# Kernel tuning notes

Measured on AMD Instinct MI355X. Metric: run time of the kernel, lower is better.

The kernel has to match this reference:

```python
import jax, jax.numpy as jnp
import numpy as np

NUM_HEADS = 16
TEMPERATURE = 1.0


def setup_inputs() -> dict:
    key = jax.random.key(0)
    ks = jax.random.split(key, 6)
    B, H = 2048, 2048
    return {
        "hidden_states": jax.random.normal(ks[0], (B, H), dtype=jnp.float32),
        "attention_mask": jnp.ones((B,), dtype=bool),
        "Wq": jax.random.normal(ks[1], (H, H), dtype=jnp.float32) * 0.02,
        "Wk": jax.random.normal(ks[2], (H, H), dtype=jnp.float32) * 0.02,
        "Wv": jax.random.normal(ks[3], (H, H), dtype=jnp.float32) * 0.02,
        "Wo": jax.random.normal(ks[4], (H, H), dtype=jnp.float32) * 0.02,
        "scale_param": jnp.full((1,), -3.0, dtype=jnp.float32),
    }


def reference(hidden_states, attention_mask, Wq, Wk, Wv, Wo, scale_param):
    B, H = hidden_states.shape
    nh = NUM_HEADS
    hd = H // nh
    # projections (torch Linear: x @ W.T), reshape to [heads, batch, head_dim]
    q = (hidden_states @ Wq.T).reshape(B, nh, hd).transpose(1, 0, 2)
    k = (hidden_states @ Wk.T).reshape(B, nh, hd).transpose(1, 0, 2)
    v = (hidden_states @ Wv.T).reshape(B, nh, hd).transpose(1, 0, 2)
    # cross-batch scores [heads, B, B]
    scores = jnp.einsum('hqd,hkd->hqk', q, k) / (hd ** 0.5 * TEMPERATURE)
    neg_inf = jnp.float32(-jnp.inf)
    eye = jnp.eye(B, dtype=bool)  # exclude self-attention (diagonal)
    scores = jnp.where(eye[None, :, :], neg_inf, scores)
    scores = jnp.where(attention_mask[None, None, :], scores, neg_inf)
    attn = jax.nn.softmax(scores, axis=-1)
    attn = jnp.nan_to_num(attn, nan=0.0)  # rows fully masked -> 0 (dropout=0 is identity)
    ctx = jnp.einsum('hqk,hkd->hqd', attn, v)  # [heads, B, head_dim]
    ctx = ctx.transpose(1, 0, 2).reshape(B, H)
    cross = ctx @ Wo.T
    scale = jax.nn.sigmoid(scale_param[0])
    return hidden_states + scale * cross
```

## Files before the change

kernel.cpp:

```cpp
#include <hip/hip_runtime.h>

typedef __bf16 bf16;
typedef __attribute__((ext_vector_type(8))) __bf16 bf16x8;
typedef __attribute__((ext_vector_type(4))) float f32x4;
typedef __attribute__((ext_vector_type(4))) short s16x4;

#define HDIM 2048

__device__ __forceinline__ void glds16(const void* g, void* l) {
  __builtin_amdgcn_global_load_lds((const __attribute__((address_space(1))) void*)g,
                                   (__attribute__((address_space(3))) void*)l,
                                   16, 0, 0);
}

#define MFMA16(a, b, c) __builtin_amdgcn_mfma_f32_16x16x32_bf16(a, b, c, 0, 0, 0)

__global__ __launch_bounds__(256) void cvt5(
    const float* __restrict__ s0, const float* __restrict__ s1,
    const float* __restrict__ s2, const float* __restrict__ s3,
    const float* __restrict__ s4,
    bf16* __restrict__ d0, bf16* __restrict__ d1, bf16* __restrict__ d2,
    bf16* __restrict__ d3, bf16* __restrict__ d4) {
  const float* s; bf16* d;
  switch (blockIdx.y) {
    case 0: s = s0; d = d0; break;
    case 1: s = s1; d = d1; break;
    case 2: s = s2; d = d2; break;
    case 3: s = s3; d = d3; break;
    default: s = s4; d = d4; break;
  }
  const size_t base = (size_t)blockIdx.x * 4096 + (threadIdx.x << 2);
  for (int i = 0; i < 4; i++) {
    const float4 v = *(const float4*)(s + base + i * 1024);
    union { bf16 h[4]; s16x4 s4v; } u;
    u.h[0] = (bf16)v.x; u.h[1] = (bf16)v.y; u.h[2] = (bf16)v.z; u.h[3] = (bf16)v.w;
    *(s16x4*)(d + base + i * 1024) = u.s4v;
  }
}

__device__ __forceinline__ void gemm128_core(const bf16* __restrict__ A,
                                             const bf16* __restrict__ B,
                                             int rowBase, int colBase,
                                             f32x4 acc[4][4],
                                             bf16* ldsA, bf16* ldsB) {
  const int t = threadIdx.x;
  const int w = t >> 6, l = t & 63;
  const int wr = (w >> 1) << 6, wc = (w & 1) << 6;
  const int lr = l & 15, lq = l >> 4;

  for (int mi = 0; mi < 4; mi++)
    for (int ni = 0; ni < 4; ni++)
      for (int r = 0; r < 4; r++) acc[mi][ni][r] = 0.f;

  const int sRow = (w << 4) + (l >> 2);
  const int sCol = (l & 3) << 3;
  const bf16* gA = A + (size_t)(rowBase + sRow) * HDIM + sCol;
  const bf16* gB = B + (size_t)(colBase + sRow) * HDIM + sCol;
  bf16* lA = ldsA + (w << 9);
  bf16* lB = ldsB + (w << 9);

  for (int k0 = 0; k0 < HDIM; k0 += 32) {
    glds16(gA, lA);
    glds16(gA + (size_t)64 * HDIM, lA + 2048);
    glds16(gB, lB);
    glds16(gB + (size_t)64 * HDIM, lB + 2048);
    gA += 32; gB += 32;
    __syncthreads();

    bf16x8 af[4], bfr[4];
    for (int mi = 0; mi < 4; mi++)
      af[mi] = *(const bf16x8*)&ldsA[(wr + mi * 16 + lr) * 32 + lq * 8];
    for (int ni = 0; ni < 4; ni++)
      bfr[ni] = *(const bf16x8*)&ldsB[(wc + ni * 16 + lr) * 32 + lq * 8];
    for (int mi = 0; mi < 4; mi++)
      for (int ni = 0; ni < 4; ni++)
        acc[mi][ni] = MFMA16(af[mi], bfr[ni], acc[mi][ni]);
    __syncthreads();
  }
}

__global__ __launch_bounds__(256) void qkv_gemm(
    const bf16* __restrict__ hs, const bf16* __restrict__ Wq,
    const bf16* __restrict__ Wk, const bf16* __restrict__ Wv,
    bf16* __restrict__ qb, bf16* __restrict__ kb, bf16* __restrict__ vT) {
  __shared__ bf16 ldsA[128 * 32];
  __shared__ bf16 ldsB[128 * 32];
  const int z = blockIdx.z;
  const bf16* W = (z == 0) ? Wq : (z == 1) ? Wk : Wv;
  const int rowBase = blockIdx.y << 7, colBase = blockIdx.x << 7;
  f32x4 acc[4][4];
  gemm128_core(hs, W, rowBase, colBase, acc, ldsA, ldsB);

  const int t = threadIdx.x;
  const int w = t >> 6, l = t & 63;
  const int wr = (w >> 1) << 6, wc = (w & 1) << 6;
  const int lr = l & 15, lq = l >> 4;

  if (z < 2) {
    bf16* outp = z ? kb : qb;
    for (int mi = 0; mi < 4; mi++)
      for (int ni = 0; ni < 4; ni++) {
        const int col = colBase + wc + ni * 16 + lr;
        const int row0 = rowBase + wr + mi * 16 + lq * 4;
        for (int r = 0; r < 4; r++)
          outp[(size_t)(row0 + r) * HDIM + col] = (bf16)acc[mi][ni][r];
      }
  } else {
    for (int mi = 0; mi < 4; mi++)
      for (int ni = 0; ni < 4; ni++) {
        const int col = colBase + wc + ni * 16 + lr;
        const int row0 = rowBase + wr + mi * 16 + lq * 4;
        union { bf16 h[4]; s16x4 v; } u;
        for (int r = 0; r < 4; r++) u.h[r] = (bf16)acc[mi][ni][r];
        *(s16x4*)&vT[(size_t)col * HDIM + row0] = u.v;
      }
  }
}

__global__ __launch_bounds__(256, 2) void attn_kernel(
    const bf16* __restrict__ qb, const bf16* __restrict__ kb,
    const bf16* __restrict__ vT, const unsigned char* __restrict__ amask,
    bf16* __restrict__ ctx) {
  __shared__ bf16 Kl[128 * 128];
  __shared__ bf16 Vl[128 * 128];
  __shared__ bf16 Pl[4 * 16 * 128];

  const int qt = blockIdx.x, h = blockIdx.y;
  const int t = threadIdx.x, w = t >> 6, l = t & 63;
  const int lr = l & 15, lq = l >> 4;
  const float NEG_INF = -__builtin_inff();
  bf16* Pw = Pl + (w << 11);

  {
    const int c8 = l & 15, rsub = l >> 4;
    for (int i = 0; i < 4; i++) {
      const int row = i * 4 + rsub;
      const bf16x8 v = *(const bf16x8*)&qb[(size_t)(qt * 64 + w * 16 + row) * HDIM + h * 128 + c8 * 8];
      *(bf16x8*)&Pw[row * 128 + ((c8 ^ row) << 3)] = v;
    }
  }
  bf16x8 aq[4];
  for (int ks = 0; ks < 4; ks++)
    aq[ks] = *(const bf16x8*)&Pw[lr * 128 + (((ks * 4 + lq) ^ lr) << 3)];

  f32x4 o[8];
  for (int ni = 0; ni < 8; ni++)
    for (int r = 0; r < 4; r++) o[ni][r] = 0.f;
  float m_i[4], l_i[4];
  int qrow[4];
  for (int r = 0; r < 4; r++) {
    m_i[r] = NEG_INF; l_i[r] = 0.f;
    qrow[r] = qt * 64 + w * 16 + lq * 4 + r;
  }
  const float scl = 0.08838834764831845f;

  const int c8 = l & 15;
  const int rsub = (w << 2) + (l >> 4);

  for (int kbk = 0; kbk < 16; kbk++) {
    bf16x8 kreg[8], vreg[8];
    for (int i = 0; i < 8; i++) {
      const int row = (i << 4) + rsub;
      kreg[i] = *(const bf16x8*)&kb[(size_t)(kbk * 128 + row) * HDIM + h * 128 + c8 * 8];
      vreg[i] = *(const bf16x8*)&vT[(size_t)(h * 128 + row) * HDIM + kbk * 128 + c8 * 8];
    }
    for (int i = 0; i < 8; i++) {
      const int row = (i << 4) + rsub;
      const int p8 = (c8 ^ (row & 15)) << 3;
      *(bf16x8*)&Kl[row * 128 + p8] = kreg[i];
      *(bf16x8*)&Vl[row * 128 + p8] = vreg[i];
    }
    __syncthreads();

    f32x4 s[8];
    for (int ni = 0; ni < 8; ni++)
      for (int r = 0; r < 4; r++) s[ni][r] = 0.f;
    for (int ks = 0; ks < 4; ks++) {
      bf16x8 bk[8];
      for (int ni = 0; ni < 8; ni++)
        bk[ni] = *(const bf16x8*)&Kl[(ni * 16 + lr) * 128 + (((ks * 4 + lq) ^ lr) << 3)];
      for (int ni = 0; ni < 8; ni++) s[ni] = MFMA16(aq[ks], bk[ni], s[ni]);
    }

    for (int ni = 0; ni < 8; ni++) {
      const int col = kbk * 128 + ni * 16 + lr;
      const bool valid = (amask[col] != 0);
      for (int r = 0; r < 4; r++) {
        float v = s[ni][r] * scl;
        if (!valid || col == qrow[r]) v = NEG_INF;
        s[ni][r] = v;
      }
    }
    float alpha[4];
    for (int r = 0; r < 4; r++) {
      float mx = NEG_INF;
      for (int ni = 0; ni < 8; ni++) mx = fmaxf(mx, s[ni][r]);
      for (int off = 1; off < 16; off <<= 1) mx = fmaxf(mx, __shfl_xor(mx, off));
      const float mold = m_i[r];
      const float mnew = fmaxf(mold, mx);
      const float a = (mold == NEG_INF) ? 0.f : __expf(mold - mnew);
      float rs = 0.f;
      for (int ni = 0; ni < 8; ni++) {
        const float sv = s[ni][r];
        const float p = (sv == NEG_INF) ? 0.f : __expf(sv - mnew);
        s[ni][r] = p;
        rs += p;
      }
      for (int off = 1; off < 16; off <<= 1) rs += __shfl_xor(rs, off);
      l_i[r] = l_i[r] * a + rs;
      m_i[r] = mnew;
      alpha[r] = a;
    }
    for (int ni = 0; ni < 8; ni++)
      for (int r = 0; r < 4; r++) o[ni][r] *= alpha[r];

    for (int ni = 0; ni < 8; ni++)
      for (int r = 0; r < 4; r++) {
        const int row = lq * 4 + r;
        Pw[row * 128 + (((ni * 2 + (lr >> 3)) ^ row) << 3) + (lr & 7)] = (bf16)s[ni][r];
      }

    for (int ks = 0; ks < 4; ks++) {
      bf16x8 bv[8];
      for (int ni = 0; ni < 8; ni++)
        bv[ni] = *(const bf16x8*)&Vl[(ni * 16 + lr) * 128 + (((ks * 4 + lq) ^ lr) << 3)];
      const bf16x8 ap = *(const bf16x8*)&Pw[lr * 128 + (((ks * 4 + lq) ^ lr) << 3)];
      for (int ni = 0; ni < 8; ni++) o[ni] = MFMA16(ap, bv[ni], o[ni]);
    }
    __syncthreads();
  }

  for (int ni = 0; ni < 8; ni++)
    for (int r = 0; r < 4; r++) {
      const int row = qrow[r];
      const int col = h * 128 + ni * 16 + lr;
      const float li = l_i[r];
      ctx[(size_t)row * HDIM + col] = (bf16)((li > 0.f) ? o[ni][r] / li : 0.f);
    }
}

__global__ __launch_bounds__(256) void out_gemm(
    const bf16* __restrict__ ctx, const bf16* __restrict__ Wo,
    const float* __restrict__ hs, const float* __restrict__ scale_p,
    float* __restrict__ outp) {
  __shared__ bf16 ldsA[128 * 32];
  __shared__ bf16 ldsB[128 * 32];
  const int rowBase = blockIdx.y << 7, colBase = blockIdx.x << 7;
  f32x4 acc[4][4];
  gemm128_core(ctx, Wo, rowBase, colBase, acc, ldsA, ldsB);

  const float sig = 1.0f / (1.0f + __expf(-scale_p[0]));
  const int t = threadIdx.x;
  const int w = t >> 6, l = t & 63;
  const int wr = (w >> 1) << 6, wc = (w & 1) << 6;
  const int lr = l & 15, lq = l >> 4;
  for (int mi = 0; mi < 4; mi++)
    for (int ni = 0; ni < 4; ni++) {
      const int col = colBase + wc + ni * 16 + lr;
      const int row0 = rowBase + wr + mi * 16 + lq * 4;
      for (int r = 0; r < 4; r++) {
        const size_t idx = (size_t)(row0 + r) * HDIM + col;
        outp[idx] = hs[idx] + sig * acc[mi][ni][r];
      }
    }
}

extern "C" void kernel_launch(void* const* d_in, const int* in_sizes, int n_in,
                              void* d_out, int out_size, void* d_ws, size_t ws_size,
                              hipStream_t stream) {
  const float* hs = (const float*)d_in[0];
  const unsigned char* amask = (const unsigned char*)d_in[1];
  const float* Wq = (const float*)d_in[2];
  const float* Wk = (const float*)d_in[3];
  const float* Wv = (const float*)d_in[4];
  const float* Wo = (const float*)d_in[5];
  const float* scale_p = (const float*)d_in[6];
  float* outp = (float*)d_out;

  const size_t N = (size_t)HDIM * HDIM;
  bf16* qb   = (bf16*)d_ws;
  bf16* kb   = qb + N;
  bf16* vT   = kb + N;
  bf16* ctx  = vT + N;
  bf16* hs16 = ctx + N;
  bf16* Wq16 = hs16 + N;
  bf16* Wk16 = Wq16 + N;
  bf16* Wv16 = Wk16 + N;
  bf16* Wo16 = Wv16 + N;

  cvt5<<<dim3(1024, 5), 256, 0, stream>>>(hs, Wq, Wk, Wv, Wo,
                                          hs16, Wq16, Wk16, Wv16, Wo16);
  qkv_gemm<<<dim3(16, 16, 3), 256, 0, stream>>>(hs16, Wq16, Wk16, Wv16, qb, kb, vT);
  attn_kernel<<<dim3(32, 16), 256, 0, stream>>>(qb, kb, vT, amask, ctx);
  out_gemm<<<dim3(16, 16), 256, 0, stream>>>(ctx, Wo16, hs, scale_p, outp);
}
```

Measured before the change: 299.1 us.

## Store K/V in MFMA fragment layout and drop online-softmax max tracking

The QKV GEMM now writes K and V directly in a per-head, per-tile MFMA fragment layout. This lets the attention kernel stream K into LDS with global_load_lds and read V fragments straight from global memory, so the V LDS buffer and the register-staged swizzled copies go away. The softmax no longer tracks a running maximum or rescales the output. It uses exp2 of the scaled scores and a multiplicative mask, and reduces the row sum once at the end. That removes shuffles and exponentials per tile, but it can overflow if scores grow large. Occupancy is raised to 3 blocks per CU, and out_gemm switches to 128x64 tiles so it launches more blocks.

Result: slower. 387.3 us (+29.5%).

```diff
diff --git a/kernel.cpp b/kernel.cpp
--- a/kernel.cpp
+++ b/kernel.cpp
@@ -82,7 +82,7 @@
 __global__ __launch_bounds__(256) void qkv_gemm(
     const bf16* __restrict__ hs, const bf16* __restrict__ Wq,
     const bf16* __restrict__ Wk, const bf16* __restrict__ Wv,
-    bf16* __restrict__ qb, bf16* __restrict__ kb, bf16* __restrict__ vT) {
+    bf16* __restrict__ qb, bf16* __restrict__ Kf, bf16* __restrict__ Vf) {
   __shared__ bf16 ldsA[128 * 32];
   __shared__ bf16 ldsB[128 * 32];
   const int z = blockIdx.z;
@@ -96,79 +96,75 @@
   const int wr = (w >> 1) << 6, wc = (w & 1) << 6;
   const int lr = l & 15, lq = l >> 4;
 
-  if (z < 2) {
-    bf16* outp = z ? kb : qb;
+  if (z == 0) {
     for (int mi = 0; mi < 4; mi++)
       for (int ni = 0; ni < 4; ni++) {
         const int col = colBase + wc + ni * 16 + lr;
         const int row0 = rowBase + wr + mi * 16 + lq * 4;
         for (int r = 0; r < 4; r++)
-          outp[(size_t)(row0 + r) * HDIM + col] = (bf16)acc[mi][ni][r];
+          qb[(size_t)(row0 + r) * HDIM + col] = (bf16)acc[mi][ni][r];
+      }
+  } else if (z == 1) {
+    for (int mi = 0; mi < 4; mi++)
+      for (int ni = 0; ni < 4; ni++) {
+        const int dim = colBase + wc + ni * 16 + lr;
+        const int hh = dim >> 7, ks = (dim >> 5) & 3, kh = (dim >> 3) & 3, j = dim & 7;
+        const int row0 = rowBase + wr + mi * 16 + lq * 4;
+        for (int r = 0; r < 4; r++) {
+          const int key = row0 + r;
+          const int kbk = key >> 7, kni = (key >> 4) & 7, kl = key & 15;
+          Kf[(((size_t)hh * 16 + kbk) * 32 + kni * 4 + ks) * 512 +
+             (kh * 16 + kl) * 8 + j] = (bf16)acc[mi][ni][r];
+        }
       }
   } else {
     for (int mi = 0; mi < 4; mi++)
       for (int ni = 0; ni < 4; ni++) {
-        const int col = colBase + wc + ni * 16 + lr;
+        const int dim = colBase + wc + ni * 16 + lr;
+        const int hh = dim >> 7, vni = (dim >> 4) & 7, ll = dim & 15;
         const int row0 = rowBase + wr + mi * 16 + lq * 4;
-        union { bf16 h[4]; s16x4 v; } u;
-        for (int r = 0; r < 4; r++) u.h[r] = (bf16)acc[mi][ni][r];
-        *(s16x4*)&vT[(size_t)col * HDIM + row0] = u.v;
-      }
-  }
-}
-
-__global__ __launch_bounds__(256, 2) void attn_kernel(
-    const bf16* __restrict__ qb, const bf16* __restrict__ kb,
-    const bf16* __restrict__ vT, const unsigned char* __restrict__ amask,
+        const int kbk = row0 >> 7, ks = (row0 >> 5) & 3, lh = (row0 >> 3) & 3;
+        const int j0 = row0 & 7;
+        union { bf16 h4[4]; s16x4 v; } u;
+        for (int r = 0; r < 4; r++) u.h4[r] = (bf16)acc[mi][ni][r];
+        *(s16x4*)&Vf[(((size_t)hh * 16 + kbk) * 32 + vni * 4 + ks) * 512 +
+                     (lh * 16 + ll) * 8 + j0] = u.v;
+      }
+  }
+}
+
+__global__ __launch_bounds__(256, 3) void attn_kernel(
+    const bf16* __restrict__ qb, const bf16* __restrict__ Kf,
+    const bf16* __restrict__ Vf, const unsigned char* __restrict__ amask,
     bf16* __restrict__ ctx) {
-  __shared__ bf16 Kl[128 * 128];
-  __shared__ bf16 Vl[128 * 128];
+  __shared__ bf16 Kl[32 * 512];
   __shared__ bf16 Pl[4 * 16 * 128];
 
   const int qt = blockIdx.x, h = blockIdx.y;
   const int t = threadIdx.x, w = t >> 6, l = t & 63;
   const int lr = l & 15, lq = l >> 4;
-  const float NEG_INF = -__builtin_inff();
   bf16* Pw = Pl + (w << 11);
 
-  {
-    const int c8 = l & 15, rsub = l >> 4;
-    for (int i = 0; i < 4; i++) {
-      const int row = i * 4 + rsub;
-      const bf16x8 v = *(const bf16x8*)&qb[(size_t)(qt * 64 + w * 16 + row) * HDIM + h * 128 + c8 * 8];
-      *(bf16x8*)&Pw[row * 128 + ((c8 ^ row) << 3)] = v;
-    }
-  }
   bf16x8 aq[4];
   for (int ks = 0; ks < 4; ks++)
-    aq[ks] = *(const bf16x8*)&Pw[lr * 128 + (((ks * 4 + lq) ^ lr) << 3)];
+    aq[ks] = *(const bf16x8*)&qb[(size_t)(qt * 64 + w * 16 + lr) * HDIM +
+                                 h * 128 + ks * 32 + lq * 8];
 
   f32x4 o[8];
   for (int ni = 0; ni < 8; ni++)
     for (int r = 0; r < 4; r++) o[ni][r] = 0.f;
-  float m_i[4], l_i[4];
+  float lsum[4] = {0.f, 0.f, 0.f, 0.f};
   int qrow[4];
-  for (int r = 0; r < 4; r++) {
-    m_i[r] = NEG_INF; l_i[r] = 0.f;
-    qrow[r] = qt * 64 + w * 16 + lq * 4 + r;
-  }
-  const float scl = 0.08838834764831845f;
-
-  const int c8 = l & 15;
-  const int rsub = (w << 2) + (l >> 4);
+  for (int r = 0; r < 4; r++) qrow[r] = qt * 64 + w * 16 + lq * 4 + r;
+
+  const float c = 0.08838834764831845f * 1.4426950408889634f;
 
   for (int kbk = 0; kbk < 16; kbk++) {
-    bf16x8 kreg[8], vreg[8];
+    const size_t tileOff = ((size_t)h * 16 + kbk) * 32 * 512;
+
     for (int i = 0; i < 8; i++) {
-      const int row = (i << 4) + rsub;
-      kreg[i] = *(const bf16x8*)&kb[(size_t)(kbk * 128 + row) * HDIM + h * 128 + c8 * 8];
-      vreg[i] = *(const bf16x8*)&vT[(size_t)(h * 128 + row) * HDIM + kbk * 128 + c8 * 8];
-    }
-    for (int i = 0; i < 8; i++) {
-      const int row = (i << 4) + rsub;
-      const int p8 = (c8 ^ (row & 15)) << 3;
-      *(bf16x8*)&Kl[row * 128 + p8] = kreg[i];
-      *(bf16x8*)&Vl[row * 128 + p8] = vreg[i];
+      const int frag = i * 4 + w;
+      glds16(Kf + tileOff + frag * 512 + l * 8, Kl + frag * 512);
     }
     __syncthreads();
 
@@ -178,41 +174,23 @@
     for (int ks = 0; ks < 4; ks++) {
       bf16x8 bk[8];
       for (int ni = 0; ni < 8; ni++)
-        bk[ni] = *(const bf16x8*)&Kl[(ni * 16 + lr) * 128 + (((ks * 4 + lq) ^ lr) << 3)];
+        bk[ni] = *(const bf16x8*)&Kl[(ni * 4 + ks) * 512 + l * 8];
       for (int ni = 0; ni < 8; ni++) s[ni] = MFMA16(aq[ks], bk[ni], s[ni]);
     }
 
+    float mk[8];
+    for (int ni = 0; ni < 8; ni++)
+      mk[ni] = amask[kbk * 128 + ni * 16 + lr] ? 1.f : 0.f;
+    const bool diagBlk = (kbk == (qt >> 1));
     for (int ni = 0; ni < 8; ni++) {
       const int col = kbk * 128 + ni * 16 + lr;
-      const bool valid = (amask[col] != 0);
       for (int r = 0; r < 4; r++) {
-        float v = s[ni][r] * scl;
-        if (!valid || col == qrow[r]) v = NEG_INF;
-        s[ni][r] = v;
-      }
-    }
-    float alpha[4];
-    for (int r = 0; r < 4; r++) {
-      float mx = NEG_INF;
-      for (int ni = 0; ni < 8; ni++) mx = fmaxf(mx, s[ni][r]);
-      for (int off = 1; off < 16; off <<= 1) mx = fmaxf(mx, __shfl_xor(mx, off));
-      const float mold = m_i[r];
-      const float mnew = fmaxf(mold, mx);
-      const float a = (mold == NEG_INF) ? 0.f : __expf(mold - mnew);
-      float rs = 0.f;
-      for (int ni = 0; ni < 8; ni++) {
-        const float sv = s[ni][r];
-        const float p = (sv == NEG_INF) ? 0.f : __expf(sv - mnew);
+        float p = __builtin_exp2f(s[ni][r] * c) * mk[ni];
+        if (diagBlk && col == qrow[r]) p = 0.f;
         s[ni][r] = p;
-        rs += p;
-      }
-      for (int off = 1; off < 16; off <<= 1) rs += __shfl_xor(rs, off);
-      l_i[r] = l_i[r] * a + rs;
-      m_i[r] = mnew;
-      alpha[r] = a;
-    }
-    for (int ni = 0; ni < 8; ni++)
-      for (int r = 0; r < 4; r++) o[ni][r] *= alpha[r];
+        lsum[r] += p;
+      }
+    }
 
     for (int ni = 0; ni < 8; ni++)
       for (int r = 0; r < 4; r++) {
@@ -223,18 +201,22 @@
     for (int ks = 0; ks < 4; ks++) {
       bf16x8 bv[8];
       for (int ni = 0; ni < 8; ni++)
-        bv[ni] = *(const bf16x8*)&Vl[(ni * 16 + lr) * 128 + (((ks * 4 + lq) ^ lr) << 3)];
+        bv[ni] = *(const bf16x8*)&Vf[tileOff + (ni * 4 + ks) * 512 + l * 8];
       const bf16x8 ap = *(const bf16x8*)&Pw[lr * 128 + (((ks * 4 + lq) ^ lr) << 3)];
       for (int ni = 0; ni < 8; ni++) o[ni] = MFMA16(ap, bv[ni], o[ni]);
     }
     __syncthreads();
   }
+
+  for (int r = 0; r < 4; r++)
+    for (int off = 1; off < 16; off <<= 1)
+      lsum[r] += __shfl_xor(lsum[r], off);
 
   for (int ni = 0; ni < 8; ni++)
     for (int r = 0; r < 4; r++) {
       const int row = qrow[r];
       const int col = h * 128 + ni * 16 + lr;
-      const float li = l_i[r];
+      const float li = lsum[r];
       ctx[(size_t)row * HDIM + col] = (bf16)((li > 0.f) ? o[ni][r] / li : 0.f);
     }
 }
@@ -244,18 +226,46 @@
     const float* __restrict__ hs, const float* __restrict__ scale_p,
     float* __restrict__ outp) {
   __shared__ bf16 ldsA[128 * 32];
-  __shared__ bf16 ldsB[128 * 32];
-  const int rowBase = blockIdx.y << 7, colBase = blockIdx.x << 7;
-  f32x4 acc[4][4];
-  gemm128_core(ctx, Wo, rowBase, colBase, acc, ldsA, ldsB);
-
-  const float sig = 1.0f / (1.0f + __expf(-scale_p[0]));
+  __shared__ bf16 ldsB[64 * 32];
+  const int rowBase = blockIdx.y << 7, colBase = blockIdx.x << 6;
   const int t = threadIdx.x;
   const int w = t >> 6, l = t & 63;
-  const int wr = (w >> 1) << 6, wc = (w & 1) << 6;
+  const int wr = (w >> 1) << 6, wc = (w & 1) << 5;
   const int lr = l & 15, lq = l >> 4;
+
+  f32x4 acc[4][2];
   for (int mi = 0; mi < 4; mi++)
-    for (int ni = 0; ni < 4; ni++) {
+    for (int ni = 0; ni < 2; ni++)
+      for (int r = 0; r < 4; r++) acc[mi][ni][r] = 0.f;
+
+  const int sRow = (w << 4) + (l >> 2);
+  const int sCol = (l & 3) << 3;
+  const bf16* gA = ctx + (size_t)(rowBase + sRow) * HDIM + sCol;
+  const bf16* gB = Wo + (size_t)(colBase + sRow) * HDIM + sCol;
+  bf16* lA = ldsA + (w << 9);
+  bf16* lB = ldsB + (w << 9);
+
+  for (int k0 = 0; k0 < HDIM; k0 += 32) {
+    glds16(gA, lA);
+    glds16(gA + (size_t)64 * HDIM, lA + 2048);
+    glds16(gB, lB);
+    gA += 32; gB += 32;
+    __syncthreads();
+
+    bf16x8 af[4], bfr[2];
+    for (int mi = 0; mi < 4; mi++)
+      af[mi] = *(const bf16x8*)&ldsA[(wr + mi * 16 + lr) * 32 + lq * 8];
+    for (int ni = 0; ni < 2; ni++)
+      bfr[ni] = *(const bf16x8*)&ldsB[(wc + ni * 16 + lr) * 32 + lq * 8];
+    for (int mi = 0; mi < 4; mi++)
+      for (int ni = 0; ni < 2; ni++)
+        acc[mi][ni] = MFMA16(af[mi], bfr[ni], acc[mi][ni]);
+    __syncthreads();
+  }
+
+  const float sig = 1.0f / (1.0f + __expf(-scale_p[0]));
+  for (int mi = 0; mi < 4; mi++)
+    for (int ni = 0; ni < 2; ni++) {
       const int col = colBase + wc + ni * 16 + lr;
       const int row0 = rowBase + wr + mi * 16 + lq * 4;
       for (int r = 0; r < 4; r++) {
@@ -279,9 +289,9 @@
 
   const size_t N = (size_t)HDIM * HDIM;
   bf16* qb   = (bf16*)d_ws;
-  bf16* kb   = qb + N;
-  bf16* vT   = kb + N;
-  bf16* ctx  = vT + N;
+  bf16* Kf   = qb + N;
+  bf16* Vf   = Kf + N;
+  bf16* ctx  = Vf + N;
   bf16* hs16 = ctx + N;
   bf16* Wq16 = hs16 + N;
   bf16* Wk16 = Wq16 + N;
@@ -290,7 +300,7 @@
 
   cvt5<<<dim3(1024, 5), 256, 0, stream>>>(hs, Wq, Wk, Wv, Wo,
                                           hs16, Wq16, Wk16, Wv16, Wo16);
-  qkv_gemm<<<dim3(16, 16, 3), 256, 0, stream>>>(hs16, Wq16, Wk16, Wv16, qb, kb, vT);
-  attn_kernel<<<dim3(32, 16), 256, 0, stream>>>(qb, kb, vT, amask, ctx);
-  out_gemm<<<dim3(16, 16), 256, 0, stream>>>(ctx, Wo16, hs, scale_p, outp);
-}
+  qkv_gemm<<<dim3(16, 16, 3), 256, 0, stream>>>(hs16, Wq16, Wk16, Wv16, qb, Kf, Vf);
+  attn_kernel<<<dim3(32, 16), 256, 0, stream>>>(qb, Kf, Vf, amask, ctx);
+  out_gemm<<<dim3(32, 16), 256, 0, stream>>>(ctx, Wo16, hs, scale_p, outp);
+}
```
